# Kernel tuning notes

Hardware: AMD Instinct MI355X
Metric: run time of the kernel (lower is better)

## Reference

```python
import jax, jax.numpy as jnp
import numpy as np

N_NODES = 1024; DEG = 24; K_NN = 12
C_S = 384; C_Z = 128; C_G = 16; N_RBF = 64
N_EDGES = N_NODES * DEG          # 24576
N_EE = N_EDGES * K_NN            # 294912 edge-edge pairs
LN_EPS = 1e-5
RBF_MIN, RBF_MAX = 0.0, 20.0


def _layernorm(x, w, b):
    m = x.mean(-1, keepdims=True)
    v = ((x - m) ** 2).mean(-1, keepdims=True)
    return (x - m) * jax.lax.rsqrt(v + LN_EPS) * w + b


def setup_inputs() -> dict:
    key = jax.random.key(0)
    ks = iter(jax.random.split(key, 40))

    def lin(i, o):
        w = jax.random.normal(next(ks), (i, o), jnp.float32) / np.sqrt(i)
        b = jax.random.normal(next(ks), (o,), jnp.float32) * 0.01
        return w, b

    node_features = jax.random.normal(next(ks), (N_NODES, C_S), jnp.float32)
    node_trans = jax.random.normal(next(ks), (N_NODES, 3), jnp.float32) * 10.0
    edge_features = jax.random.normal(next(ks), (N_EDGES, C_Z), jnp.float32)

    # edge_index sorted by destination (column 1), fixed in-degree DEG per node
    rng = np.random.default_rng(0)
    dst = np.repeat(np.arange(N_NODES), DEG)
    src = rng.integers(0, N_NODES, size=N_EDGES)
    edge_index = jnp.asarray(np.stack([src, dst]), jnp.int32)

    # edge-edge kNN graph: each edge paired with K_NN other edges sharing the
    # same destination node (mirrors knn_graph(..., batch=sorted_edge_index[1]))
    t = np.arange(N_EDGES)
    base = (t // DEG) * DEG
    off = t % DEG
    nbr = base[:, None] + (off[:, None] + 1 + np.arange(K_NN)[None, :]) % DEG  # [E,K]
    edge_edge_index = jnp.asarray(
        np.stack([nbr.reshape(-1), np.repeat(t, K_NN)]), jnp.int32)  # [2, N_EE]

    ln_w = jnp.ones((C_Z,), jnp.float32); ln_b = jnp.zeros((C_Z,), jnp.float32)
    wl_w, wl_b = lin(C_S, C_G)
    wr_w, wr_b = lin(C_S, C_G)
    ep_w, ep_b = lin(C_Z, C_Z)
    eg_w, eg_b = lin(C_Z, C_Z)
    dg_w, dg_b = lin(C_G * C_G, C_Z)
    dp_w, dp_b = lin(N_RBF, C_Z)
    lno_w = jnp.ones((C_Z,), jnp.float32); lno_b = jnp.zeros((C_Z,), jnp.float32)
    lo_w, lo_b = lin(C_Z, C_Z)
    og_w, og_b = lin(C_Z, C_Z)

    return dict(node_features=node_features, node_trans=node_trans,
                edge_features=edge_features,
                ln_w=ln_w, ln_b=ln_b, wl_w=wl_w, wl_b=wl_b, wr_w=wr_w, wr_b=wr_b,
                ep_w=ep_w, ep_b=ep_b, eg_w=eg_w, eg_b=eg_b,
                dg_w=dg_w, dg_b=dg_b, dp_w=dp_w, dp_b=dp_b,
                lno_w=lno_w, lno_b=lno_b, lo_w=lo_w, lo_b=lo_b,
                og_w=og_w, og_b=og_b,
                edge_index=edge_index, edge_edge_index=edge_edge_index)


def reference(node_features, node_trans, edge_features,
              ln_w, ln_b, wl_w, wl_b, wr_w, wr_b,
              ep_w, ep_b, eg_w, eg_b, dg_w, dg_b, dp_w, dp_b,
              lno_w, lno_b, lo_w, lo_b, og_w, og_b,
              edge_index, edge_edge_index):
    eps = 1e-8
    src = edge_index[0]
    eei0, eei1 = edge_edge_index[0], edge_edge_index[1]
    n1 = src[eei1]  # source node of target edge of each pair
    n2 = src[eei0]  # source node of source edge of each pair

    ef = _layernorm(edge_features, ln_w, ln_b)            # [E, c_z]
    nl = node_features @ wl_w + wl_b                      # [N, c_g]
    nr = node_features @ wr_w + wr_b                      # [N, c_g]

    # per-pair outer product, flattened: [N_EE, c_g*c_g]
    e3 = (nl[n1][:, :, None] * nr[n2][:, None, :]).reshape(-1, C_G * C_G)
    gate3 = e3 @ dg_w + dg_b                              # [N_EE, c_z]

    d = jnp.linalg.norm(node_trans[n1] - node_trans[n2] + eps, axis=-1)
    mu = jnp.linspace(RBF_MIN, RBF_MAX, N_RBF)
    sigma = (RBF_MAX - RBF_MIN) / N_RBF
    rbf = jnp.exp(-(((d[:, None] - mu) / sigma) ** 2))    # [N_EE, num_rbf]
    e3f = jax.nn.sigmoid(gate3) * (rbf @ dp_w + dp_b)

    e2 = jax.nn.sigmoid(ef @ eg_w + eg_b) * (ef @ ep_w + ep_b)  # [E, c_z]
    upd = e2[eei0] * e3f                                  # [N_EE, c_z]
    upd = jax.ops.segment_sum(upd, eei0, num_segments=N_EDGES)  # [E, c_z]

    upd = _layernorm(upd, lno_w, lno_b) @ lo_w + lo_b
    upd = upd * jax.nn.sigmoid(ef @ og_w + og_b)
    return upd
```

## Files before the change

kernel.cpp:

```cpp
#include <hip/hip_runtime.h>
#include <math.h>

#define N_NODES 1024
#define DEG     24
#define K_NN    12
#define C_S     384
#define C_Z     128
#define C_G     16
#define N_RBF   64
#define N_EDGES (N_NODES*DEG)

typedef short short8 __attribute__((ext_vector_type(8)));
typedef float f32x4  __attribute__((ext_vector_type(4)));

__device__ __forceinline__ float sigf(float x) {
  return __builtin_amdgcn_rcpf(1.f + __expf(-x));
}

__device__ __forceinline__ short f2b(float x) {
  union { float f; unsigned u; } v; v.f = x;
  unsigned r = v.u + 0x7FFFu + ((v.u >> 16) & 1u);
  return (short)(r >> 16);
}
__device__ __forceinline__ float b2f(short s) {
  union { unsigned u; float f; } v; v.u = ((unsigned)(unsigned short)s) << 16;
  return v.f;
}

__global__ __launch_bounds__(256) void k_prep(
    const float* __restrict__ nf, const float* __restrict__ wl_w, const float* __restrict__ wl_b,
    const float* __restrict__ wr_w, const float* __restrict__ wr_b,
    const float* __restrict__ dg_w,
    const float* __restrict__ eg, const float* __restrict__ ep,
    const float* __restrict__ og, const float* __restrict__ lo,
    const float* __restrict__ dp_w,
    short* __restrict__ nlB, short* __restrict__ At,
    short* __restrict__ wT, short* __restrict__ dpT)
{
  __shared__ float rows[4][C_S];
  __shared__ float nrv[4][C_G];
  __shared__ float tb[32][33];
  int b = blockIdx.x, t = threadIdx.x;
  if (b < 256) {
    for (int v = t; v < 4*C_S; v += 256) rows[v/C_S][v%C_S] = nf[(size_t)b*4*C_S + v];
    __syncthreads();
    {
      int nd = t >> 6, lt = t & 63;
      int c = lt >> 1, jseg = lt & 1, cc = c & 15;
      const float* w = (c < 16) ? wl_w : wr_w;
      float acc = 0.f;
      #pragma unroll 8
      for (int j = jseg*192; j < jseg*192 + 192; ++j) acc += rows[nd][j] * w[j*C_G + cc];
      acc += __shfl_xor(acc, 1);
      if (jseg == 0) {
        float v = acc + ((c < 16) ? wl_b[cc] : wr_b[cc]);
        if (c < 16) nlB[(b*4 + nd)*C_G + cc] = f2b(v);
        else nrv[nd][cc] = v;
      }
    }
    __syncthreads();
    {
      int c2 = t & 127, ih = t >> 7;
      float a4[4][8];
      #pragma unroll
      for (int nd = 0; nd < 4; ++nd)
        #pragma unroll
        for (int q = 0; q < 8; ++q) a4[nd][q] = 0.f;
      for (int j = 0; j < C_G; ++j) {
        float w8[8];
        #pragma unroll
        for (int q = 0; q < 8; ++q) w8[q] = dg_w[(size_t)((ih*8 + q)*C_G + j)*C_Z + c2];
        #pragma unroll
        for (int nd = 0; nd < 4; ++nd) {
          float nv = nrv[nd][j];
          #pragma unroll
          for (int q = 0; q < 8; ++q) a4[nd][q] += nv * w8[q];
        }
      }
      #pragma unroll
      for (int nd = 0; nd < 4; ++nd) {
        short8 o8;
        #pragma unroll
        for (int q = 0; q < 8; ++q) o8[q] = f2b(a4[nd][q]);
        *(short8*)&At[(size_t)(b*4 + nd)*2048 + c2*16 + ih*8] = o8;
      }
    }
    return;
  }
  if (b < 320) {
    int bb = b - 256;
    int w = bb >> 4, tile = bb & 15, bi = tile >> 2, bj = tile & 3;
    const float* src = (w == 0) ? eg : (w == 1) ? ep : (w == 2) ? og : lo;
    short* dst = wT + w * 16384;
    int c = t & 31, r0 = t >> 5;
    #pragma unroll
    for (int p = 0; p < 4; ++p) { int r = r0 + p*8; tb[r][c] = src[(bi*32 + r)*128 + bj*32 + c]; }
    __syncthreads();
    #pragma unroll
    for (int p = 0; p < 4; ++p) { int r = r0 + p*8; dst[(bj*32 + r)*128 + bi*32 + c] = f2b(tb[c][r]); }
    return;
  }
  {
    int c2 = t & 127, rh = t >> 7;
    for (int r = rh*36; r < rh*36 + 36; ++r)
      dpT[c2*72 + r] = (r < 64) ? f2b(dp_w[r*128 + c2]) : (short)0;
  }
}

__global__ __launch_bounds__(256) void k_gates2(
    const float* __restrict__ efin, const float* __restrict__ ln_w, const float* __restrict__ ln_b,
    const short* __restrict__ wT,
    const float* __restrict__ eg_b, const float* __restrict__ ep_b, const float* __restrict__ og_b,
    float* __restrict__ e2, short* __restrict__ ogs)
{
  __shared__ short xn[16*136];
  int t = threadIdx.x;
  int ebase = blockIdx.x * 16;
  {
    int el = t >> 4, sub = t & 15, c0 = sub*8;
    float x[8];
    size_t ein = (size_t)(ebase + el) * C_Z + c0;
    float4 v0 = *(const float4*)(efin + ein);
    float4 v1 = *(const float4*)(efin + ein + 4);
    x[0]=v0.x; x[1]=v0.y; x[2]=v0.z; x[3]=v0.w;
    x[4]=v1.x; x[5]=v1.y; x[6]=v1.z; x[7]=v1.w;
    float s = 0.f;
    #pragma unroll
    for (int q = 0; q < 8; ++q) s += x[q];
    s += __shfl_xor(s,1); s += __shfl_xor(s,2); s += __shfl_xor(s,4); s += __shfl_xor(s,8);
    float mean = s * (1.f/128.f);
    float vs = 0.f;
    #pragma unroll
    for (int q = 0; q < 8; ++q) { float d = x[q]-mean; vs += d*d; }
    vs += __shfl_xor(vs,1); vs += __shfl_xor(vs,2); vs += __shfl_xor(vs,4); vs += __shfl_xor(vs,8);
    float rstd = rsqrtf(vs*(1.f/128.f) + 1e-5f);
    short8 o;
    #pragma unroll
    for (int q = 0; q < 8; ++q)
      o[q] = f2b((x[q]-mean)*rstd*ln_w[c0+q] + ln_b[c0+q]);
    *(short8*)&xn[el*136 + c0] = o;
  }
  __syncthreads();
  int wv = t >> 6, lane = t & 63, col = lane & 15, grp = lane >> 4;
  short8 a[4];
  #pragma unroll
  for (int ks = 0; ks < 4; ++ks)
    a[ks] = *(const short8*)&xn[col*136 + ks*32 + grp*8];
  #pragma unroll
  for (int hh = 0; hh < 2; ++hh) {
    int ch = col + 16*(wv*2 + hh);
    f32x4 aE = (f32x4){0.f,0.f,0.f,0.f}, aP = aE, aO = aE;
    #pragma unroll
    for (int ks = 0; ks < 4; ++ks) {
      aE = __builtin_amdgcn_mfma_f32_16x16x32_bf16(
          a[ks], *(const short8*)(wT + (size_t)ch*128 + ks*32 + grp*8), aE, 0, 0, 0);
      aP = __builtin_amdgcn_mfma_f32_16x16x32_bf16(
          a[ks], *(const short8*)(wT + 16384 + (size_t)ch*128 + ks*32 + grp*8), aP, 0, 0, 0);
      aO = __builtin_amdgcn_mfma_f32_16x16x32_bf16(
          a[ks], *(const short8*)(wT + 32768 + (size_t)ch*128 + ks*32 + grp*8), aO, 0, 0, 0);
    }
    float egb = eg_b[ch], epb = ep_b[ch], ogb = og_b[ch];
    #pragma unroll
    for (int r = 0; r < 4; ++r) {
      size_t e = (size_t)(ebase + grp*4 + r);
      e2[e*C_Z + ch]  = sigf(aE[r] + egb) * (aP[r] + epb);
      ogs[e*C_Z + ch] = f2b(sigf(aO[r] + ogb));
    }
  }
}

__global__ __launch_bounds__(256) void k_pairs2(
    const int* __restrict__ eidx, const float* __restrict__ pos,
    const short* __restrict__ nlB, const short* __restrict__ At, const short* __restrict__ dpTg,
    const float* __restrict__ dg_b, const float* __restrict__ dp_b,
    const float* __restrict__ e2, const float* __restrict__ lno_w, const float* __restrict__ lno_b,
    short* __restrict__ Un)
{
  __shared__ float p4[DEG][4];
  __shared__ int   s24[DEG];
  __shared__ short nlb[DEG*C_G];
  int t = threadIdx.x;
  int g = blockIdx.x / 6, sub = blockIdx.x - g*6;
  if (t < DEG) {
    int s = eidx[g*DEG + t];
    s24[t] = s;
    p4[t][0] = pos[s*3+0]; p4[t][1] = pos[s*3+1]; p4[t][2] = pos[s*3+2]; p4[t][3] = 0.f;
  }
  __syncthreads();
  for (int v = t; v < DEG*C_G; v += 256)
    nlb[v] = nlB[s24[v>>4]*C_G + (v & 15)];
  __syncthreads();

  int wv = t >> 6, lane = t & 63, col = lane & 15, grp = lane >> 4;
  int o = sub*4 + wv;
  size_t e = (size_t)g*DEG + o;

  float dgb[8], dpb[8];
  #pragma unroll
  for (int q = 0; q < 8; ++q) { int c = col+16*q; dgb[q] = dg_b[c]; dpb[q] = dp_b[c]; }
  const float RS = 3.2f, MUS = 20.f/63.f;

  int n2 = s24[o];
  int o2 = o - 1 - col; if (o2 < 0) o2 += DEG;
  bool vk = (col < K_NN);
  float d;
  {
    float dx = p4[o2][0]-p4[o][0]+1e-8f;
    float dy = p4[o2][1]-p4[o][1]+1e-8f;
    float dz = p4[o2][2]-p4[o][2]+1e-8f;
    d = vk ? sqrtf(dx*dx+dy*dy+dz*dz) : 1.0e6f;
  }
  short8 zz = {0,0,0,0,0,0,0,0};
  short8 a_nl = zz;
  if (vk && grp < 2) a_nl = *(const short8*)&nlb[o2*C_G + grp*8];
  short8 a_r0, a_r1;
  #pragma unroll
  for (int j = 0; j < 8; ++j) {
    float z0 = (d - (float)(grp*8 + j)*MUS)*RS;
    float z1 = (d - (float)(32 + grp*8 + j)*MUS)*RS;
    a_r0[j] = f2b(__expf(-z0*z0));
    a_r1[j] = f2b(__expf(-z1*z1));
  }
  const short8* Ab = (const short8*)(At + (size_t)n2*2048);
  float v1 = 0.f, v2 = 0.f;
  #pragma unroll
  for (int cb = 0; cb < 8; ++cb) {
    f32x4 accg = (f32x4){dgb[cb],dgb[cb],dgb[cb],dgb[cb]};
    f32x4 accd = (f32x4){dpb[cb],dpb[cb],dpb[cb],dpb[cb]};
    short8 b = (grp < 2) ? Ab[(col+16*cb)*2 + grp] : zz;
    accg = __builtin_amdgcn_mfma_f32_16x16x32_bf16(a_nl, b, accg, 0, 0, 0);
    const short* dbase = dpTg + (col+16*cb)*72 + grp*8;
    accd = __builtin_amdgcn_mfma_f32_16x16x32_bf16(a_r0, *(const short8*)dbase,      accd, 0, 0, 0);
    accd = __builtin_amdgcn_mfma_f32_16x16x32_bf16(a_r1, *(const short8*)(dbase+32), accd, 0, 0, 0);
    float sacc = 0.f;
    #pragma unroll
    for (int r = 0; r < 4; ++r)
      sacc += sigf(accg[r]) * accd[r];
    sacc = (grp == 3) ? 0.f : sacc;
    sacc += __shfl_xor(sacc, 16); sacc += __shfl_xor(sacc, 32);
    v1 = (cb == grp)     ? sacc : v1;
    v2 = (cb == grp + 4) ? sacc : v2;
  }
  v1 *= e2[e*C_Z + lane];
  v2 *= e2[e*C_Z + 64 + lane];
  float s = v1 + v2;
  s += __shfl_xor(s,1); s += __shfl_xor(s,2); s += __shfl_xor(s,4);
  s += __shfl_xor(s,8); s += __shfl_xor(s,16); s += __shfl_xor(s,32);
  float mean = s * (1.f/128.f);
  float d1 = v1 - mean, d2 = v2 - mean;
  float vsum = d1*d1 + d2*d2;
  vsum += __shfl_xor(vsum,1); vsum += __shfl_xor(vsum,2); vsum += __shfl_xor(vsum,4);
  vsum += __shfl_xor(vsum,8); vsum += __shfl_xor(vsum,16); vsum += __shfl_xor(vsum,32);
  float rstd = rsqrtf(vsum*(1.f/128.f) + 1e-5f);
  Un[e*C_Z + lane]      = f2b(d1*rstd*lno_w[lane]      + lno_b[lane]);
  Un[e*C_Z + 64 + lane] = f2b(d2*rstd*lno_w[64 + lane] + lno_b[64 + lane]);
}

__global__ __launch_bounds__(256) void k_out3(
    const short* __restrict__ Un, const short* __restrict__ wTlo, const float* __restrict__ lo_b,
    const short* __restrict__ ogs, float* __restrict__ out)
{
  int t = threadIdx.x, wv = t >> 6, lane = t & 63, col = lane & 15, grp = lane >> 4;
  int ebase = blockIdx.x * 16;
  short8 ua[4];
  #pragma unroll
  for (int ks = 0; ks < 4; ++ks)
    ua[ks] = *(const short8*)(Un + (size_t)(ebase + col)*C_Z + ks*32 + grp*8);
  #pragma unroll
  for (int hh = 0; hh < 2; ++hh) {
    int ch = col + 16*(wv*2 + hh);
    f32x4 oacc = (f32x4){0.f,0.f,0.f,0.f};
    #pragma unroll
    for (int ks = 0; ks < 4; ++ks)
      oacc = __builtin_amdgcn_mfma_f32_16x16x32_bf16(
          ua[ks], *(const short8*)(wTlo + (size_t)ch*128 + ks*32 + grp*8), oacc, 0, 0, 0);
    float lob = lo_b[ch];
    #pragma unroll
    for (int r = 0; r < 4; ++r) {
      size_t e = (size_t)(ebase + grp*4 + r);
      out[e*C_Z + ch] = (oacc[r] + lob) * b2f(ogs[e*C_Z + ch]);
    }
  }
}

extern "C" void kernel_launch(void* const* d_in, const int* in_sizes, int n_in,
                              void* d_out, int out_size, void* d_ws, size_t ws_size,
                              hipStream_t stream)
{
  const float* nf    = (const float*)d_in[0];
  const float* pos   = (const float*)d_in[1];
  const float* efin  = (const float*)d_in[2];
  const float* ln_w  = (const float*)d_in[3];
  const float* ln_b  = (const float*)d_in[4];
  const float* wl_w  = (const float*)d_in[5];
  const float* wl_b  = (const float*)d_in[6];
  const float* wr_w  = (const float*)d_in[7];
  const float* wr_b  = (const float*)d_in[8];
  const float* ep_w  = (const float*)d_in[9];
  const float* ep_b  = (const float*)d_in[10];
  const float* eg_w  = (const float*)d_in[11];
  const float* eg_b  = (const float*)d_in[12];
  const float* dg_w  = (const float*)d_in[13];
  const float* dg_b  = (const float*)d_in[14];
  const float* dp_w  = (const float*)d_in[15];
  const float* dp_b  = (const float*)d_in[16];
  const float* lno_w = (const float*)d_in[17];
  const float* lno_b = (const float*)d_in[18];
  const float* lo_w  = (const float*)d_in[19];
  const float* lo_b  = (const float*)d_in[20];
  const float* og_w  = (const float*)d_in[21];
  const float* og_b  = (const float*)d_in[22];
  const int*   eidx  = (const int*)d_in[23];

  float* ws   = (float*)d_ws;
  short* nlBw = (short*)(ws + 0);
  short* dpTw = (short*)(ws + 8192);
  short* wTw  = (short*)(ws + 16384);
  short* Atw  = (short*)(ws + 49152);
  float* e2w  = ws + 1097728;
  short* ogw  = (short*)(ws + 4243456);
  short* Unw  = (short*)(ws + 5816320);
  float* outp = (float*)d_out;

  k_prep  <<<321, 256, 0, stream>>>(nf, wl_w, wl_b, wr_w, wr_b, dg_w,
                                    eg_w, ep_w, og_w, lo_w, dp_w,
                                    nlBw, Atw, wTw, dpTw);
  k_gates2<<<1536, 256, 0, stream>>>(efin, ln_w, ln_b, wTw, eg_b, ep_b, og_b, e2w, ogw);
  k_pairs2<<<6144, 256, 0, stream>>>(eidx, pos, nlBw, Atw, dpTw, dg_b, dp_b,
                                     e2w, lno_w, lno_b, Unw);
  k_out3  <<<1536, 256, 0, stream>>>(Unw, wTw + 49152, lo_b, ogw, outp);
}
```

Measured before the change: 103.9 us.

## Merge gates and pairs kernels into one launch, move e2 multiply and LN to output

Combines the edge-gate kernel and the pair kernel into a single grid with branches on block index, so the two independent stages run concurrently and one launch is dropped. To remove the dependency of the pair stage on e2, the pair stage now writes the raw per-edge sums S in fp32. The e2 multiply and the output LayerNorm move into the final output kernel. This removes a serialization point, but the S intermediate doubles in size compared with the bf16 Un buffer and the output kernel now reads more data.

```diff
diff --git a/kernel.cpp b/kernel.cpp
--- a/kernel.cpp
+++ b/kernel.cpp
@@ -107,165 +107,194 @@
   }
 }
 
-__global__ __launch_bounds__(256) void k_gates2(
+__global__ __launch_bounds__(256) void k_gp(
+    const int* __restrict__ eidx, const float* __restrict__ pos,
+    const short* __restrict__ nlB, const short* __restrict__ At, const short* __restrict__ dpTg,
+    const float* __restrict__ dg_b, const float* __restrict__ dp_b,
+    float* __restrict__ S,
     const float* __restrict__ efin, const float* __restrict__ ln_w, const float* __restrict__ ln_b,
     const short* __restrict__ wT,
     const float* __restrict__ eg_b, const float* __restrict__ ep_b, const float* __restrict__ og_b,
     float* __restrict__ e2, short* __restrict__ ogs)
 {
-  __shared__ short xn[16*136];
-  int t = threadIdx.x;
-  int ebase = blockIdx.x * 16;
-  {
-    int el = t >> 4, sub = t & 15, c0 = sub*8;
-    float x[8];
-    size_t ein = (size_t)(ebase + el) * C_Z + c0;
-    float4 v0 = *(const float4*)(efin + ein);
-    float4 v1 = *(const float4*)(efin + ein + 4);
-    x[0]=v0.x; x[1]=v0.y; x[2]=v0.z; x[3]=v0.w;
-    x[4]=v1.x; x[5]=v1.y; x[6]=v1.z; x[7]=v1.w;
-    float s = 0.f;
-    #pragma unroll
-    for (int q = 0; q < 8; ++q) s += x[q];
-    s += __shfl_xor(s,1); s += __shfl_xor(s,2); s += __shfl_xor(s,4); s += __shfl_xor(s,8);
-    float mean = s * (1.f/128.f);
-    float vs = 0.f;
-    #pragma unroll
-    for (int q = 0; q < 8; ++q) { float d = x[q]-mean; vs += d*d; }
-    vs += __shfl_xor(vs,1); vs += __shfl_xor(vs,2); vs += __shfl_xor(vs,4); vs += __shfl_xor(vs,8);
-    float rstd = rsqrtf(vs*(1.f/128.f) + 1e-5f);
-    short8 o;
-    #pragma unroll
-    for (int q = 0; q < 8; ++q)
-      o[q] = f2b((x[q]-mean)*rstd*ln_w[c0+q] + ln_b[c0+q]);
-    *(short8*)&xn[el*136 + c0] = o;
-  }
-  __syncthreads();
-  int wv = t >> 6, lane = t & 63, col = lane & 15, grp = lane >> 4;
-  short8 a[4];
-  #pragma unroll
-  for (int ks = 0; ks < 4; ++ks)
-    a[ks] = *(const short8*)&xn[col*136 + ks*32 + grp*8];
-  #pragma unroll
-  for (int hh = 0; hh < 2; ++hh) {
-    int ch = col + 16*(wv*2 + hh);
-    f32x4 aE = (f32x4){0.f,0.f,0.f,0.f}, aP = aE, aO = aE;
-    #pragma unroll
-    for (int ks = 0; ks < 4; ++ks) {
-      aE = __builtin_amdgcn_mfma_f32_16x16x32_bf16(
-          a[ks], *(const short8*)(wT + (size_t)ch*128 + ks*32 + grp*8), aE, 0, 0, 0);
-      aP = __builtin_amdgcn_mfma_f32_16x16x32_bf16(
-          a[ks], *(const short8*)(wT + 16384 + (size_t)ch*128 + ks*32 + grp*8), aP, 0, 0, 0);
-      aO = __builtin_amdgcn_mfma_f32_16x16x32_bf16(
-          a[ks], *(const short8*)(wT + 32768 + (size_t)ch*128 + ks*32 + grp*8), aO, 0, 0, 0);
-    }
-    float egb = eg_b[ch], epb = ep_b[ch], ogb = og_b[ch];
-    #pragma unroll
-    for (int r = 0; r < 4; ++r) {
-      size_t e = (size_t)(ebase + grp*4 + r);
-      e2[e*C_Z + ch]  = sigf(aE[r] + egb) * (aP[r] + epb);
-      ogs[e*C_Z + ch] = f2b(sigf(aO[r] + ogb));
-    }
-  }
-}
-
-__global__ __launch_bounds__(256) void k_pairs2(
-    const int* __restrict__ eidx, const float* __restrict__ pos,
-    const short* __restrict__ nlB, const short* __restrict__ At, const short* __restrict__ dpTg,
-    const float* __restrict__ dg_b, const float* __restrict__ dp_b,
-    const float* __restrict__ e2, const float* __restrict__ lno_w, const float* __restrict__ lno_b,
-    short* __restrict__ Un)
-{
   __shared__ float p4[DEG][4];
   __shared__ int   s24[DEG];
   __shared__ short nlb[DEG*C_G];
-  int t = threadIdx.x;
-  int g = blockIdx.x / 6, sub = blockIdx.x - g*6;
-  if (t < DEG) {
-    int s = eidx[g*DEG + t];
-    s24[t] = s;
-    p4[t][0] = pos[s*3+0]; p4[t][1] = pos[s*3+1]; p4[t][2] = pos[s*3+2]; p4[t][3] = 0.f;
-  }
-  __syncthreads();
-  for (int v = t; v < DEG*C_G; v += 256)
-    nlb[v] = nlB[s24[v>>4]*C_G + (v & 15)];
-  __syncthreads();
-
+  __shared__ short xn[16*136];
+  int b = blockIdx.x, t = threadIdx.x;
   int wv = t >> 6, lane = t & 63, col = lane & 15, grp = lane >> 4;
-  int o = sub*4 + wv;
-  size_t e = (size_t)g*DEG + o;
-
-  float dgb[8], dpb[8];
-  #pragma unroll
-  for (int q = 0; q < 8; ++q) { int c = col+16*q; dgb[q] = dg_b[c]; dpb[q] = dp_b[c]; }
-  const float RS = 3.2f, MUS = 20.f/63.f;
-
-  int n2 = s24[o];
-  int o2 = o - 1 - col; if (o2 < 0) o2 += DEG;
-  bool vk = (col < K_NN);
-  float d;
+
+  if (b < 6144) {
+    int g = b / 6, sub = b - g*6;
+    if (t < DEG) {
+      int s = eidx[g*DEG + t];
+      s24[t] = s;
+      p4[t][0] = pos[s*3+0]; p4[t][1] = pos[s*3+1]; p4[t][2] = pos[s*3+2]; p4[t][3] = 0.f;
+    }
+    __syncthreads();
+    for (int v = t; v < DEG*C_G; v += 256)
+      nlb[v] = nlB[s24[v>>4]*C_G + (v & 15)];
+    __syncthreads();
+
+    int o = sub*4 + wv;
+    size_t e = (size_t)g*DEG + o;
+
+    float dgb[8], dpb[8];
+    #pragma unroll
+    for (int q = 0; q < 8; ++q) { int c = col+16*q; dgb[q] = dg_b[c]; dpb[q] = dp_b[c]; }
+    const float RS = 3.2f, MUS = 20.f/63.f;
+
+    int n2 = s24[o];
+    int o2 = o - 1 - col; if (o2 < 0) o2 += DEG;
+    bool vk = (col < K_NN);
+    float d;
+    {
+      float dx = p4[o2][0]-p4[o][0]+1e-8f;
+      float dy = p4[o2][1]-p4[o][1]+1e-8f;
+      float dz = p4[o2][2]-p4[o][2]+1e-8f;
+      d = vk ? sqrtf(dx*dx+dy*dy+dz*dz) : 1.0e6f;
+    }
+    short8 zz = {0,0,0,0,0,0,0,0};
+    short8 a_nl = zz;
+    if (vk && grp < 2) a_nl = *(const short8*)&nlb[o2*C_G + grp*8];
+    short8 a_r0, a_r1;
+    #pragma unroll
+    for (int j = 0; j < 8; ++j) {
+      float z0 = (d - (float)(grp*8 + j)*MUS)*RS;
+      float z1 = (d - (float)(32 + grp*8 + j)*MUS)*RS;
+      a_r0[j] = f2b(__expf(-z0*z0));
+      a_r1[j] = f2b(__expf(-z1*z1));
+    }
+    const short8* Ab = (const short8*)(At + (size_t)n2*2048);
+    float v1 = 0.f, v2 = 0.f;
+    #pragma unroll
+    for (int cb = 0; cb < 8; ++cb) {
+      f32x4 accg = (f32x4){0.f,0.f,0.f,0.f};
+      f32x4 accd = (f32x4){0.f,0.f,0.f,0.f};
+      short8 bb = (grp < 2) ? Ab[(col+16*cb)*2 + grp] : zz;
+      accg = __builtin_amdgcn_mfma_f32_16x16x32_bf16(a_nl, bb, accg, 0, 0, 0);
+      const short* dbase = dpTg + (col+16*cb)*72 + grp*8;
+      accd = __builtin_amdgcn_mfma_f32_16x16x32_bf16(a_r0, *(const short8*)dbase,      accd, 0, 0, 0);
+      accd = __builtin_amdgcn_mfma_f32_16x16x32_bf16(a_r1, *(const short8*)(dbase+32), accd, 0, 0, 0);
+      float sacc = 0.f;
+      #pragma unroll
+      for (int r = 0; r < 4; ++r)
+        sacc += sigf(accg[r] + dgb[cb]) * (accd[r] + dpb[cb]);
+      sacc = (grp == 3) ? 0.f : sacc;
+      sacc += __shfl_xor(sacc, 16); sacc += __shfl_xor(sacc, 32);
+      v1 = (cb == grp)     ? sacc : v1;
+      v2 = (cb == grp + 4) ? sacc : v2;
+    }
+    S[e*C_Z + lane]      = v1;
+    S[e*C_Z + 64 + lane] = v2;
+    return;
+  }
+
   {
-    float dx = p4[o2][0]-p4[o][0]+1e-8f;
-    float dy = p4[o2][1]-p4[o][1]+1e-8f;
-    float dz = p4[o2][2]-p4[o][2]+1e-8f;
-    d = vk ? sqrtf(dx*dx+dy*dy+dz*dz) : 1.0e6f;
-  }
-  short8 zz = {0,0,0,0,0,0,0,0};
-  short8 a_nl = zz;
-  if (vk && grp < 2) a_nl = *(const short8*)&nlb[o2*C_G + grp*8];
-  short8 a_r0, a_r1;
-  #pragma unroll
-  for (int j = 0; j < 8; ++j) {
-    float z0 = (d - (float)(grp*8 + j)*MUS)*RS;
-    float z1 = (d - (float)(32 + grp*8 + j)*MUS)*RS;
-    a_r0[j] = f2b(__expf(-z0*z0));
-    a_r1[j] = f2b(__expf(-z1*z1));
-  }
-  const short8* Ab = (const short8*)(At + (size_t)n2*2048);
-  float v1 = 0.f, v2 = 0.f;
-  #pragma unroll
-  for (int cb = 0; cb < 8; ++cb) {
-    f32x4 accg = (f32x4){dgb[cb],dgb[cb],dgb[cb],dgb[cb]};
-    f32x4 accd = (f32x4){dpb[cb],dpb[cb],dpb[cb],dpb[cb]};
-    short8 b = (grp < 2) ? Ab[(col+16*cb)*2 + grp] : zz;
-    accg = __builtin_amdgcn_mfma_f32_16x16x32_bf16(a_nl, b, accg, 0, 0, 0);
-    const short* dbase = dpTg + (col+16*cb)*72 + grp*8;
-    accd = __builtin_amdgcn_mfma_f32_16x16x32_bf16(a_r0, *(const short8*)dbase,      accd, 0, 0, 0);
-    accd = __builtin_amdgcn_mfma_f32_16x16x32_bf16(a_r1, *(const short8*)(dbase+32), accd, 0, 0, 0);
-    float sacc = 0.f;
-    #pragma unroll
-    for (int r = 0; r < 4; ++r)
-      sacc += sigf(accg[r]) * accd[r];
-    sacc = (grp == 3) ? 0.f : sacc;
-    sacc += __shfl_xor(sacc, 16); sacc += __shfl_xor(sacc, 32);
-    v1 = (cb == grp)     ? sacc : v1;
-    v2 = (cb == grp + 4) ? sacc : v2;
-  }
-  v1 *= e2[e*C_Z + lane];
-  v2 *= e2[e*C_Z + 64 + lane];
-  float s = v1 + v2;
-  s += __shfl_xor(s,1); s += __shfl_xor(s,2); s += __shfl_xor(s,4);
-  s += __shfl_xor(s,8); s += __shfl_xor(s,16); s += __shfl_xor(s,32);
-  float mean = s * (1.f/128.f);
-  float d1 = v1 - mean, d2 = v2 - mean;
-  float vsum = d1*d1 + d2*d2;
-  vsum += __shfl_xor(vsum,1); vsum += __shfl_xor(vsum,2); vsum += __shfl_xor(vsum,4);
-  vsum += __shfl_xor(vsum,8); vsum += __shfl_xor(vsum,16); vsum += __shfl_xor(vsum,32);
-  float rstd = rsqrtf(vsum*(1.f/128.f) + 1e-5f);
-  Un[e*C_Z + lane]      = f2b(d1*rstd*lno_w[lane]      + lno_b[lane]);
-  Un[e*C_Z + 64 + lane] = f2b(d2*rstd*lno_w[64 + lane] + lno_b[64 + lane]);
-}
-
-__global__ __launch_bounds__(256) void k_out3(
-    const short* __restrict__ Un, const short* __restrict__ wTlo, const float* __restrict__ lo_b,
+    int ebase = (b - 6144) * 16;
+    {
+      int el = t >> 4, sub = t & 15, c0 = sub*8;
+      float x[8];
+      size_t ein = (size_t)(ebase + el) * C_Z + c0;
+      float4 v0 = *(const float4*)(efin + ein);
+      float4 v1 = *(const float4*)(efin + ein + 4);
+      x[0]=v0.x; x[1]=v0.y; x[2]=v0.z; x[3]=v0.w;
+      x[4]=v1.x; x[5]=v1.y; x[6]=v1.z; x[7]=v1.w;
+      float s = 0.f;
+      #pragma unroll
+      for (int q = 0; q < 8; ++q) s += x[q];
+      s += __shfl_xor(s,1); s += __shfl_xor(s,2); s += __shfl_xor(s,4); s += __shfl_xor(s,8);
+      float mean = s * (1.f/128.f);
+      float vs = 0.f;
+      #pragma unroll
+      for (int q = 0; q < 8; ++q) { float dd = x[q]-mean; vs += dd*dd; }
+      vs += __shfl_xor(vs,1); vs += __shfl_xor(vs,2); vs += __shfl_xor(vs,4); vs += __shfl_xor(vs,8);
+      float rstd = rsqrtf(vs*(1.f/128.f) + 1e-5f);
+      short8 o;
+      #pragma unroll
+      for (int q = 0; q < 8; ++q)
+        o[q] = f2b((x[q]-mean)*rstd*ln_w[c0+q] + ln_b[c0+q]);
+      *(short8*)&xn[el*136 + c0] = o;
+    }
+    __syncthreads();
+    short8 a[4];
+    #pragma unroll
+    for (int ks = 0; ks < 4; ++ks)
+      a[ks] = *(const short8*)&xn[col*136 + ks*32 + grp*8];
+    #pragma unroll
+    for (int hh = 0; hh < 2; ++hh) {
+      int ch = col + 16*(wv*2 + hh);
+      f32x4 aE = (f32x4){0.f,0.f,0.f,0.f}, aP = aE, aO = aE;
+      #pragma unroll
+      for (int ks = 0; ks < 4; ++ks) {
+        aE = __builtin_amdgcn_mfma_f32_16x16x32_bf16(
+            a[ks], *(const short8*)(wT + (size_t)ch*128 + ks*32 + grp*8), aE, 0, 0, 0);
+        aP = __builtin_amdgcn_mfma_f32_16x16x32_bf16(
+            a[ks], *(const short8*)(wT + 16384 + (size_t)ch*128 + ks*32 + grp*8), aP, 0, 0, 0);
+        aO = __builtin_amdgcn_mfma_f32_16x16x32_bf16(
+            a[ks], *(const short8*)(wT + 32768 + (size_t)ch*128 + ks*32 + grp*8), aO, 0, 0, 0);
+      }
+      float egb = eg_b[ch], epb = ep_b[ch], ogb = og_b[ch];
+      #pragma unroll
+      for (int r = 0; r < 4; ++r) {
+        size_t e = (size_t)(ebase + grp*4 + r);
+        e2[e*C_Z + ch]  = sigf(aE[r] + egb) * (aP[r] + epb);
+        ogs[e*C_Z + ch] = f2b(sigf(aO[r] + ogb));
+      }
+    }
+  }
+}
+
+__global__ __launch_bounds__(256) void k_out4(
+    const float* __restrict__ S, const float* __restrict__ e2,
+    const float* __restrict__ lno_w, const float* __restrict__ lno_b,
+    const short* __restrict__ wTlo, const float* __restrict__ lo_b,
     const short* __restrict__ ogs, float* __restrict__ out)
 {
   int t = threadIdx.x, wv = t >> 6, lane = t & 63, col = lane & 15, grp = lane >> 4;
   int ebase = blockIdx.x * 16;
+  size_t e = (size_t)(ebase + col);
+
+  float u[32];
+  float s = 0.f;
+  #pragma unroll
+  for (int ks = 0; ks < 4; ++ks) {
+    size_t base = e*C_Z + ks*32 + grp*8;
+    float4 s0 = *(const float4*)(S + base);
+    float4 s1 = *(const float4*)(S + base + 4);
+    float4 g0 = *(const float4*)(e2 + base);
+    float4 g1 = *(const float4*)(e2 + base + 4);
+    u[ks*8+0] = s0.x*g0.x; u[ks*8+1] = s0.y*g0.y; u[ks*8+2] = s0.z*g0.z; u[ks*8+3] = s0.w*g0.w;
+    u[ks*8+4] = s1.x*g1.x; u[ks*8+5] = s1.y*g1.y; u[ks*8+6] = s1.z*g1.z; u[ks*8+7] = s1.w*g1.w;
+    #pragma unroll
+    for (int j = 0; j < 8; ++j) s += u[ks*8+j];
+  }
+  s += __shfl_xor(s, 16); s += __shfl_xor(s, 32);
+  float mean = s * (1.f/128.f);
+  float vs = 0.f;
+  #pragma unroll
+  for (int q = 0; q < 32; ++q) { float dd = u[q]-mean; vs += dd*dd; }
+  vs += __shfl_xor(vs, 16); vs += __shfl_xor(vs, 32);
+  float rstd = rsqrtf(vs*(1.f/128.f) + 1e-5f);
+
   short8 ua[4];
   #pragma unroll
-  for (int ks = 0; ks < 4; ++ks)
-    ua[ks] = *(const short8*)(Un + (size_t)(ebase + col)*C_Z + ks*32 + grp*8);
+  for (int ks = 0; ks < 4; ++ks) {
+    int cb = ks*32 + grp*8;
+    float4 w0 = *(const float4*)(lno_w + cb);
+    float4 w1 = *(const float4*)(lno_w + cb + 4);
+    float4 b0 = *(const float4*)(lno_b + cb);
+    float4 b1 = *(const float4*)(lno_b + cb + 4);
+    ua[ks][0] = f2b((u[ks*8+0]-mean)*rstd*w0.x + b0.x);
+    ua[ks][1] = f2b((u[ks*8+1]-mean)*rstd*w0.y + b0.y);
+    ua[ks][2] = f2b((u[ks*8+2]-mean)*rstd*w0.z + b0.z);
+    ua[ks][3] = f2b((u[ks*8+3]-mean)*rstd*w0.w + b0.w);
+    ua[ks][4] = f2b((u[ks*8+4]-mean)*rstd*w1.x + b1.x);
+    ua[ks][5] = f2b((u[ks*8+5]-mean)*rstd*w1.y + b1.y);
+    ua[ks][6] = f2b((u[ks*8+6]-mean)*rstd*w1.z + b1.z);
+    ua[ks][7] = f2b((u[ks*8+7]-mean)*rstd*w1.w + b1.w);
+  }
+
   #pragma unroll
   for (int hh = 0; hh < 2; ++hh) {
     int ch = col + 16*(wv*2 + hh);
@@ -277,8 +306,8 @@
     float lob = lo_b[ch];
     #pragma unroll
     for (int r = 0; r < 4; ++r) {
-      size_t e = (size_t)(ebase + grp*4 + r);
-      out[e*C_Z + ch] = (oacc[r] + lob) * b2f(ogs[e*C_Z + ch]);
+      size_t eo = (size_t)(ebase + grp*4 + r);
+      out[eo*C_Z + ch] = (oacc[r] + lob) * b2f(ogs[eo*C_Z + ch]);
     }
   }
 }
@@ -319,14 +348,13 @@
   short* Atw  = (short*)(ws + 49152);
   float* e2w  = ws + 1097728;
   short* ogw  = (short*)(ws + 4243456);
-  short* Unw  = (short*)(ws + 5816320);
+  float* Sw   = ws + 5816320;
   float* outp = (float*)d_out;
 
-  k_prep  <<<321, 256, 0, stream>>>(nf, wl_w, wl_b, wr_w, wr_b, dg_w,
-                                    eg_w, ep_w, og_w, lo_w, dp_w,
-                                    nlBw, Atw, wTw, dpTw);
-  k_gates2<<<1536, 256, 0, stream>>>(efin, ln_w, ln_b, wTw, eg_b, ep_b, og_b, e2w, ogw);
-  k_pairs2<<<6144, 256, 0, stream>>>(eidx, pos, nlBw, Atw, dpTw, dg_b, dp_b,
-                                     e2w, lno_w, lno_b, Unw);
-  k_out3  <<<1536, 256, 0, stream>>>(Unw, wTw + 49152, lo_b, ogw, outp);
-}
+  k_prep<<<321, 256, 0, stream>>>(nf, wl_w, wl_b, wr_w, wr_b, dg_w,
+                                  eg_w, ep_w, og_w, lo_w, dp_w,
+                                  nlBw, Atw, wTw, dpTw);
+  k_gp  <<<7680, 256, 0, stream>>>(eidx, pos, nlBw, Atw, dpTw, dg_b, dp_b, Sw,
+                                   efin, ln_w, ln_b, wTw, eg_b, ep_b, og_b, e2w, ogw);
+  k_out4<<<1536, 256, 0, stream>>>(Sw, e2w, lno_w, lno_b, wTw + 49152, lo_b, ogw, outp);
+}
```

Measured after the change: 104.5 us. About the same (+0.6%).
